# Performance work log

Hardware: AMD Instinct MI355X
Metric: run time of the kernel (lower is better)

## Reference

```python
import jax, jax.numpy as jnp
import numpy as np

DIM = 3072
HEADS = 24
HEAD_DIM = 128
INNER = HEADS * HEAD_DIM
EPS = 1e-6
B, IMG_LEN, TXT_LEN = 1, 2048, 512
S = IMG_LEN + TXT_LEN


def setup_inputs() -> dict:
    key = jax.random.key(0)
    ks = jax.random.split(key, 16)
    w = lambda k, shp: (jax.random.normal(k, shp, dtype=jnp.float32) * 0.02)
    return {
        "x": jax.random.normal(ks[0], (B, IMG_LEN, DIM), dtype=jnp.float32),
        "ctx": jax.random.normal(ks[1], (B, TXT_LEN, DIM), dtype=jnp.float32),
        "rope_cos": jax.random.uniform(ks[2], (S, HEAD_DIM), dtype=jnp.float32),
        "rope_sin": jax.random.uniform(ks[3], (S, HEAD_DIM), dtype=jnp.float32),
        "wq": w(ks[4], (INNER, DIM)),
        "wk": w(ks[5], (INNER, DIM)),
        "wv": w(ks[6], (INNER, DIM)),
        "gq": jnp.ones((HEAD_DIM,), jnp.float32),
        "gk": jnp.ones((HEAD_DIM,), jnp.float32),
        "wo": w(ks[7], (DIM, INNER)),
        "awq": w(ks[8], (INNER, DIM)),
        "awk": w(ks[9], (INNER, DIM)),
        "awv": w(ks[10], (INNER, DIM)),
        "agq": jnp.ones((HEAD_DIM,), jnp.float32),
        "agk": jnp.ones((HEAD_DIM,), jnp.float32),
        "awo": w(ks[11], (DIM, INNER)),
    }


def _rms_norm(t, g):
    # t: [b, s, h, d]; normalize over last dim
    var = jnp.mean(t * t, axis=-1, keepdims=True)
    return t * jax.lax.rsqrt(var + EPS) * g


def _heads(t):
    # [b, s, h*d] -> [b, s, h, d]
    b, s, _ = t.shape
    return t.reshape(b, s, HEADS, HEAD_DIM)


def _apply_rope(t, cos, sin):
    # t: [b, s, h, d]; cos/sin: [s, d] interleaved-pair layout (diffusers Flux style)
    b, s, h, d = t.shape
    x = t.reshape(b, s, h, d // 2, 2)
    rot = jnp.stack([-x[..., 1], x[..., 0]], axis=-1).reshape(b, s, h, d)
    c = cos[None, :, None, :]
    si = sin[None, :, None, :]
    return t * c + rot * si


def reference(x, ctx, rope_cos, rope_sin, wq, wk, wv, gq, gk, wo,
              awq, awk, awv, agq, agk, awo):
    # image-stream QKV + per-head RMSNorm on q,k
    q = _rms_norm(_heads(x @ wq.T), gq)
    k = _rms_norm(_heads(x @ wk.T), gk)
    v = _heads(x @ wv.T)
    # context-stream QKV
    qc = _rms_norm(_heads(ctx @ awq.T), agq)
    kc = _rms_norm(_heads(ctx @ awk.T), agk)
    vc = _heads(ctx @ awv.T)
    # joint streams: [ctx, img] ordering (out[:, :txt_len] is context)
    q = jnp.concatenate([qc, q], axis=1)
    k = jnp.concatenate([kc, k], axis=1)
    v = jnp.concatenate([vc, v], axis=1)
    q = _apply_rope(q, rope_cos, rope_sin)
    k = _apply_rope(k, rope_cos, rope_sin)
    # SDPA
    scale = 1.0 / jnp.sqrt(jnp.float32(HEAD_DIM))
    scores = jnp.einsum('bqhd,bkhd->bhqk', q, k) * scale
    probs = jax.nn.softmax(scores, axis=-1)
    out = jnp.einsum('bhqk,bkhd->bqhd', probs, v)
    out = out.reshape(out.shape[0], out.shape[1], INNER)
    img_out = out[:, TXT_LEN:] @ wo.T
    txt_out = out[:, :TXT_LEN] @ awo.T
    return (img_out, txt_out)
```

## Files before the change

kernel.cpp:

```cpp
#include <hip/hip_runtime.h>
#include <hip/hip_bf16.h>

#define DIMC 3072
#define NHEADS 24
#define HD 128
#define SEQ 2560
#define TXTLEN 512
#define IMGLEN 2048

using short8 = __attribute__((ext_vector_type(8))) short;
using f32x4  = __attribute__((ext_vector_type(4))) float;

static __device__ __forceinline__ float bf2f(unsigned short u) {
    unsigned v = ((unsigned)u) << 16;
    return __builtin_bit_cast(float, v);
}
static __device__ __forceinline__ unsigned short f2bf(float f) {
    unsigned u = __builtin_bit_cast(unsigned, f);
    return (unsigned short)((u + 0x7FFFu + ((u >> 16) & 1u)) >> 16);
}
static __device__ __forceinline__ void gload16(const void* g, void* l) {
    __builtin_amdgcn_global_load_lds((const __attribute__((address_space(1))) unsigned int*)g,
                                     (__attribute__((address_space(3))) unsigned int*)l,
                                     16, 0, 0);
}

struct C2 { const float* src[2]; size_t n8[2]; unsigned short* dst[2]; };
__global__ __launch_bounds__(256)
void castk2(C2 a)
{
    const int which = blockIdx.y;
    const size_t i = (size_t)blockIdx.x * 256 + threadIdx.x;
    if (i >= a.n8[which]) return;
    const float* in = a.src[which];
    unsigned short* out = a.dst[which];
    const float4 av = *reinterpret_cast<const float4*>(in + i * 8);
    const float4 bv = *reinterpret_cast<const float4*>(in + i * 8 + 4);
    short8 o;
    o[0] = (short)f2bf(av.x); o[1] = (short)f2bf(av.y);
    o[2] = (short)f2bf(av.z); o[3] = (short)f2bf(av.w);
    o[4] = (short)f2bf(bv.x); o[5] = (short)f2bf(bv.y);
    o[6] = (short)f2bf(bv.z); o[7] = (short)f2bf(bv.w);
    *reinterpret_cast<short8*>(out + i * 8) = o;
}

struct W8 { const float* src[8]; };
__global__ __launch_bounds__(256)
void castw(W8 a, unsigned short* __restrict__ dstbase, int n8, size_t wsz)
{
    const int i = blockIdx.x * 256 + threadIdx.x;
    if (i >= n8) return;
    const float* in = a.src[blockIdx.y];
    unsigned short* out = dstbase + (size_t)blockIdx.y * wsz;
    const float4 av = *reinterpret_cast<const float4*>(in + (size_t)i * 8);
    const float4 bv = *reinterpret_cast<const float4*>(in + (size_t)i * 8 + 4);
    short8 o;
    o[0] = (short)f2bf(av.x); o[1] = (short)f2bf(av.y);
    o[2] = (short)f2bf(av.z); o[3] = (short)f2bf(av.w);
    o[4] = (short)f2bf(bv.x); o[5] = (short)f2bf(bv.y);
    o[6] = (short)f2bf(bv.z); o[7] = (short)f2bf(bv.w);
    *reinterpret_cast<short8*>(out + (size_t)i * 8) = o;
}

struct QkvArgs {
    const unsigned short* A;
    const unsigned short* w0[3];
    const unsigned short* w1[3];
    unsigned short* c[3];
};

__global__ __launch_bounds__(256)
void gemm_qkv(QkvArgs args)
{
    __shared__ unsigned short As[3][128 * 32];
    __shared__ unsigned short Bs[3][128 * 32];

    const int bid = blockIdx.x;
    const int swz = (bid & 7) * 180 + (bid >> 3);
    const int bm = swz % 20;
    int bn = swz / 20;
    const int which = bn / 24; bn -= which * 24;

    const int rowbase = bm * 128, colbase = bn * 128;
    const unsigned short* __restrict__ A = args.A;
    const unsigned short* __restrict__ W = (rowbase < TXTLEN) ? args.w0[which] : args.w1[which];
    unsigned short* __restrict__ C = args.c[which];

    const int t = threadIdx.x, w = t >> 6, l = t & 63;
    const int lr = l & 15, lk = l >> 4;
    const int wr = (w >> 1) * 64, wc = (w & 1) * 64;

    f32x4 acc[4][4] = {};

    const int ssl = ((l & 3) ^ ((l >> 3) & 3)) * 8;
    const unsigned short* Ag = A + (size_t)(rowbase + w * 32 + (l >> 2)) * DIMC + ssl;
    const unsigned short* Wg = W + (size_t)(colbase + w * 32 + (l >> 2)) * DIMC + ssl;

    auto STAGE = [&](int buf, int k0) {
        gload16(Ag + k0,             &As[buf][w * 1024]);
        gload16(Ag + 16 * DIMC + k0, &As[buf][w * 1024 + 512]);
        gload16(Wg + k0,             &Bs[buf][w * 1024]);
        gload16(Wg + 16 * DIMC + k0, &Bs[buf][w * 1024 + 512]);
    };

    constexpr int NIT = DIMC / 32;
    STAGE(0, 0);
    STAGE(1, 32);

    const int rsl = (lk ^ ((lr >> 1) & 3)) * 8;
    int buf = 0;
    for (int it = 0; it < NIT; ++it) {
        asm volatile("s_waitcnt vmcnt(4)" ::: "memory");
        __builtin_amdgcn_s_barrier();
        asm volatile("" ::: "memory");

        {
            const int k2 = (it + 2 < NIT) ? (it + 2) : (NIT - 1);
            int b2 = buf + 2; if (b2 >= 3) b2 -= 3;
            STAGE(b2, k2 * 32);
        }

        short8 af[4], bf[4];
#pragma unroll
        for (int m = 0; m < 4; ++m)
            af[m] = *reinterpret_cast<const short8*>(&As[buf][(wr + m * 16 + lr) * 32 + rsl]);
#pragma unroll
        for (int n = 0; n < 4; ++n)
            bf[n] = *reinterpret_cast<const short8*>(&Bs[buf][(wc + n * 16 + lr) * 32 + rsl]);

        __builtin_amdgcn_s_setprio(1);
#pragma unroll
        for (int m = 0; m < 4; ++m)
#pragma unroll
            for (int n = 0; n < 4; ++n)
                acc[m][n] = __builtin_amdgcn_mfma_f32_16x16x32_bf16(af[m], bf[n], acc[m][n], 0, 0, 0);
        __builtin_amdgcn_s_setprio(0);

        buf = (buf + 1 == 3) ? 0 : buf + 1;
    }

#pragma unroll
    for (int m = 0; m < 4; ++m) {
#pragma unroll
        for (int r = 0; r < 4; ++r) {
            const int row = rowbase + wr + m * 16 + lk * 4 + r;
            unsigned short* crow = C + (size_t)row * DIMC + colbase + wc;
#pragma unroll
            for (int n = 0; n < 4; ++n)
                crow[n * 16 + lr] = f2bf(acc[m][n][r]);
        }
    }
}

__global__ __launch_bounds__(256)
void gemm_out(const unsigned short* __restrict__ A, const unsigned short* __restrict__ W0,
              const unsigned short* __restrict__ W1, float* __restrict__ Ctxt,
              float* __restrict__ Cimg)
{
    __shared__ unsigned short As[3][128 * 32];
    __shared__ unsigned short Bs[3][128 * 32];

    const int bid = blockIdx.x;
    const int swz = (bid & 7) * 60 + (bid >> 3);
    const int bm = swz % 20;
    const int bn = swz / 20;

    const int rowbase = bm * 128, colbase = bn * 128;
    const unsigned short* __restrict__ W = (rowbase < TXTLEN) ? W0 : W1;

    const int t = threadIdx.x, w = t >> 6, l = t & 63;
    const int lr = l & 15, lk = l >> 4;
    const int wr = (w >> 1) * 64, wc = (w & 1) * 64;

    f32x4 acc[4][4] = {};

    const int ssl = ((l & 3) ^ ((l >> 3) & 3)) * 8;
    const unsigned short* Ag = A + (size_t)(rowbase + w * 32 + (l >> 2)) * DIMC + ssl;
    const unsigned short* Wg = W + (size_t)(colbase + w * 32 + (l >> 2)) * DIMC + ssl;

    auto STAGE = [&](int buf, int k0) {
        gload16(Ag + k0,             &As[buf][w * 1024]);
        gload16(Ag + 16 * DIMC + k0, &As[buf][w * 1024 + 512]);
        gload16(Wg + k0,             &Bs[buf][w * 1024]);
        gload16(Wg + 16 * DIMC + k0, &Bs[buf][w * 1024 + 512]);
    };

    constexpr int NIT = DIMC / 32;
    STAGE(0, 0);
    STAGE(1, 32);

    const int rsl = (lk ^ ((lr >> 1) & 3)) * 8;
    int buf = 0;
    for (int it = 0; it < NIT; ++it) {
        asm volatile("s_waitcnt vmcnt(4)" ::: "memory");
        __builtin_amdgcn_s_barrier();
        asm volatile("" ::: "memory");

        {
            const int k2 = (it + 2 < NIT) ? (it + 2) : (NIT - 1);
            int b2 = buf + 2; if (b2 >= 3) b2 -= 3;
            STAGE(b2, k2 * 32);
        }

        short8 af[4], bf[4];
#pragma unroll
        for (int m = 0; m < 4; ++m)
            af[m] = *reinterpret_cast<const short8*>(&As[buf][(wr + m * 16 + lr) * 32 + rsl]);
#pragma unroll
        for (int n = 0; n < 4; ++n)
            bf[n] = *reinterpret_cast<const short8*>(&Bs[buf][(wc + n * 16 + lr) * 32 + rsl]);

        __builtin_amdgcn_s_setprio(1);
#pragma unroll
        for (int m = 0; m < 4; ++m)
#pragma unroll
            for (int n = 0; n < 4; ++n)
                acc[m][n] = __builtin_amdgcn_mfma_f32_16x16x32_bf16(af[m], bf[n], acc[m][n], 0, 0, 0);
        __builtin_amdgcn_s_setprio(0);

        buf = (buf + 1 == 3) ? 0 : buf + 1;
    }

    float* Cb; int rloc;
    if (rowbase < TXTLEN) { Cb = Ctxt; rloc = rowbase; }
    else                  { Cb = Cimg; rloc = rowbase - TXTLEN; }
#pragma unroll
    for (int m = 0; m < 4; ++m) {
#pragma unroll
        for (int r = 0; r < 4; ++r) {
            const int row = rloc + wr + m * 16 + lk * 4 + r;
            float* crow = Cb + (size_t)row * DIMC + colbase + wc;
#pragma unroll
            for (int n = 0; n < 4; ++n)
                crow[n * 16 + lr] = acc[m][n][r];
        }
    }
}

__global__ __launch_bounds__(256)
void normrope(unsigned short* __restrict__ Q, unsigned short* __restrict__ K,
              const float* __restrict__ gq, const float* __restrict__ gk,
              const float* __restrict__ agq, const float* __restrict__ agk,
              const float* __restrict__ rc, const float* __restrict__ rs)
{
    const int wid  = (blockIdx.x << 2) + (threadIdx.x >> 6);
    const int lane = threadIdx.x & 63;
    const int s = wid / NHEADS, h = wid - s * NHEADS;
    const bool img = (s >= TXTLEN);
    const float* gq_ = img ? gq : agq;
    const float* gk_ = img ? gk : agk;

    const size_t base = (size_t)s * DIMC + h * HD + lane * 2;
    const float2 c2  = *reinterpret_cast<const float2*>(rc + (size_t)s * HD + lane * 2);
    const float2 s2  = *reinterpret_cast<const float2*>(rs + (size_t)s * HD + lane * 2);
    const float2 gqv = *reinterpret_cast<const float2*>(gq_ + lane * 2);
    const float2 gkv = *reinterpret_cast<const float2*>(gk_ + lane * 2);

    {
        unsigned pr = *reinterpret_cast<unsigned*>(Q + base);
        float vx = bf2f((unsigned short)(pr & 0xffff));
        float vy = bf2f((unsigned short)(pr >> 16));
        float ss = vx * vx + vy * vy;
#pragma unroll
        for (int off = 1; off < 64; off <<= 1) ss += __shfl_xor(ss, off);
        const float rr = rsqrtf(ss * (1.f / HD) + 1e-6f);
        const float txv = vx * rr * gqv.x, tyv = vy * rr * gqv.y;
        const float qs = 0.08838834764831845f;
        const float ox = (txv * c2.x - tyv * s2.x) * qs;
        const float oy = (tyv * c2.y + txv * s2.y) * qs;
        *reinterpret_cast<unsigned*>(Q + base) = (unsigned)f2bf(ox) | ((unsigned)f2bf(oy) << 16);
    }
    {
        unsigned pr = *reinterpret_cast<unsigned*>(K + base);
        float vx = bf2f((unsigned short)(pr & 0xffff));
        float vy = bf2f((unsigned short)(pr >> 16));
        float ss = vx * vx + vy * vy;
#pragma unroll
        for (int off = 1; off < 64; off <<= 1) ss += __shfl_xor(ss, off);
        const float rr = rsqrtf(ss * (1.f / HD) + 1e-6f);
        const float txv = vx * rr * gkv.x, tyv = vy * rr * gkv.y;
        const float ox = txv * c2.x - tyv * s2.x;
        const float oy = tyv * c2.y + txv * s2.y;
        *reinterpret_cast<unsigned*>(K + base) = (unsigned)f2bf(ox) | ((unsigned)f2bf(oy) << 16);
    }
}

__global__ __launch_bounds__(256)
void transpose_v(const unsigned short* __restrict__ V, unsigned short* __restrict__ Vt)
{
    __shared__ unsigned short Ts[64][136];
    const int kt = blockIdx.x, h = blockIdx.y;
    const int t = threadIdx.x;
#pragma unroll
    for (int p = 0; p < 4; ++p) {
        const int row = p * 16 + (t >> 4);
        const int col = (t & 15) * 8;
        *reinterpret_cast<short8*>(&Ts[row][col]) =
            *reinterpret_cast<const short8*>(V + (size_t)(kt * 64 + row) * DIMC + h * HD + col);
    }
    __syncthreads();
    const int d = t >> 1, kh = t & 1;
    unsigned short* dst = Vt + (size_t)h * HD * SEQ + (size_t)d * SEQ + kt * 64 + kh * 32;
#pragma unroll
    for (int j4 = 0; j4 < 4; ++j4) {
        short8 o;
#pragma unroll
        for (int j = 0; j < 8; ++j) o[j] = (short)Ts[kh * 32 + j4 * 8 + j][d];
        *reinterpret_cast<short8*>(dst + j4 * 8) = o;
    }
}

__global__ __launch_bounds__(512)
void attn_mfma(const unsigned short* __restrict__ Q, const unsigned short* __restrict__ K,
               const unsigned short* __restrict__ Vt, unsigned short* __restrict__ O)
{
    __shared__ unsigned short Ks[2][64 * 128];
    __shared__ unsigned short Vs[2][128 * 64];
    __shared__ unsigned short Ps[8][16 * 64];

    const int bid = blockIdx.x;
    const int swz = (bid & 7) * 60 + (bid >> 3);
    const int bq = swz % 20;
    const int h  = swz / 20;

    const int t = threadIdx.x, w = t >> 6, l = t & 63;
    const int lr = l & 15, lk = l >> 4;
    const int q0 = bq * 128 + w * 16;

    short8 qf[4];
#pragma unroll
    for (int kk = 0; kk < 4; ++kk)
        qf[kk] = *reinterpret_cast<const short8*>(
            Q + (size_t)(q0 + lr) * DIMC + h * HD + kk * 32 + lk * 8);

    f32x4 oacc[8] = {};
    float mrow[4] = {-1e30f, -1e30f, -1e30f, -1e30f};
    float lrow[4] = {};

    const unsigned short* Kg[2];
    const unsigned short* Vg[2];
#pragma unroll
    for (int i = 0; i < 2; ++i) {
        const int kr = w * 8 + i * 4 + (l >> 4);
        Kg[i] = K + (size_t)kr * DIMC + h * HD + (((l & 15) ^ (kr & 7)) * 8);
        const int vr = w * 16 + i * 8 + (l >> 3);
        Vg[i] = Vt + (size_t)h * HD * SEQ + (size_t)vr * SEQ + (((l & 7) ^ (vr & 7)) * 8);
    }

    auto STAGE = [&](int buf, int kv0) {
#pragma unroll
        for (int i = 0; i < 2; ++i) {
            gload16(Kg[i] + (size_t)kv0 * DIMC, &Ks[buf][(w * 8 + i * 4) * 128]);
            gload16(Vg[i] + kv0,                &Vs[buf][(w * 16 + i * 8) * 64]);
        }
    };

    STAGE(0, 0);

    constexpr int NT = SEQ / 64;
    for (int kt = 0; kt < NT; ++kt) {
        const int buf = kt & 1;
        __syncthreads();
        if (kt + 1 < NT) STAGE(buf ^ 1, (kt + 1) * 64);

        f32x4 sf[4] = {};
        __builtin_amdgcn_s_setprio(1);
#pragma unroll
        for (int nf = 0; nf < 4; ++nf) {
            const int row = nf * 16 + lr;
            const int sw = (row & 7) << 3;
#pragma unroll
            for (int kk = 0; kk < 4; ++kk) {
                short8 bfr = *reinterpret_cast<const short8*>(
                    &Ks[buf][row * 128 + ((kk * 32 + lk * 8) ^ sw)]);
                sf[nf] = __builtin_amdgcn_mfma_f32_16x16x32_bf16(qf[kk], bfr, sf[nf], 0, 0, 0);
            }
        }
        __builtin_amdgcn_s_setprio(0);

        float mxr[4];
#pragma unroll
        for (int r = 0; r < 4; ++r) {
            float mx = fmaxf(fmaxf(sf[0][r], sf[1][r]), fmaxf(sf[2][r], sf[3][r]));
#pragma unroll
            for (int off = 1; off < 16; off <<= 1) mx = fmaxf(mx, __shfl_xor(mx, off));
            mxr[r] = mx;
        }
        const float need = fmaxf(fmaxf(mxr[0] - mrow[0], mxr[1] - mrow[1]),
                                 fmaxf(mxr[2] - mrow[2], mxr[3] - mrow[3]));
        if (!__all(need <= 8.0f)) {
#pragma unroll
            for (int r = 0; r < 4; ++r) {
                const float mn = fmaxf(mrow[r], mxr[r]);
                const float alpha = __expf(mrow[r] - mn);
                mrow[r] = mn;
                lrow[r] *= alpha;
#pragma unroll
                for (int nf = 0; nf < 8; ++nf) oacc[nf][r] *= alpha;
            }
        }
#pragma unroll
        for (int r = 0; r < 4; ++r) {
            float ps = 0.f;
#pragma unroll
            for (int nf = 0; nf < 4; ++nf) {
                const float p = __expf(sf[nf][r] - mrow[r]);
                sf[nf][r] = p;
                ps += p;
            }
#pragma unroll
            for (int off = 1; off < 16; off <<= 1) ps += __shfl_xor(ps, off);
            lrow[r] += ps;
        }

#pragma unroll
        for (int r = 0; r < 4; ++r) {
            const int prow = lk * 4 + r;
            const int sw = (prow & 7) << 3;
#pragma unroll
            for (int nf = 0; nf < 4; ++nf) {
                const int col = nf * 16 + lr;
                Ps[w][prow * 64 + (col ^ sw)] = f2bf(sf[nf][r]);
            }
        }

        __builtin_amdgcn_s_setprio(1);
#pragma unroll
        for (int ks = 0; ks < 2; ++ks) {
            short8 pa = *reinterpret_cast<const short8*>(
                &Ps[w][lr * 64 + ((ks * 32 + lk * 8) ^ ((lr & 7) << 3))]);
#pragma unroll
            for (int nf = 0; nf < 8; ++nf) {
                const int vrow = nf * 16 + lr;
                short8 vf = *reinterpret_cast<const short8*>(
                    &Vs[buf][vrow * 64 + ((ks * 32 + lk * 8) ^ ((vrow & 7) << 3))]);
                oacc[nf] = __builtin_amdgcn_mfma_f32_16x16x32_bf16(pa, vf, oacc[nf], 0, 0, 0);
            }
        }
        __builtin_amdgcn_s_setprio(0);
    }

    float inv[4];
#pragma unroll
    for (int r = 0; r < 4; ++r) inv[r] = 1.f / lrow[r];
#pragma unroll
    for (int nf = 0; nf < 8; ++nf)
#pragma unroll
        for (int r = 0; r < 4; ++r)
            O[(size_t)(q0 + lk * 4 + r) * DIMC + h * HD + nf * 16 + lr] = f2bf(oacc[nf][r] * inv[r]);
}

extern "C" void kernel_launch(void* const* d_in, const int* in_sizes, int n_in,
                              void* d_out, int out_size, void* d_ws, size_t ws_size,
                              hipStream_t stream)
{
    const float* x    = (const float*)d_in[0];
    const float* ctx  = (const float*)d_in[1];
    const float* rc   = (const float*)d_in[2];
    const float* rs   = (const float*)d_in[3];
    const float* wq   = (const float*)d_in[4];
    const float* wk   = (const float*)d_in[5];
    const float* wv   = (const float*)d_in[6];
    const float* gq   = (const float*)d_in[7];
    const float* gk   = (const float*)d_in[8];
    const float* wo   = (const float*)d_in[9];
    const float* awq  = (const float*)d_in[10];
    const float* awk  = (const float*)d_in[11];
    const float* awv  = (const float*)d_in[12];
    const float* agq  = (const float*)d_in[13];
    const float* agk  = (const float*)d_in[14];
    const float* awo  = (const float*)d_in[15];

    unsigned short* wsp = (unsigned short*)d_ws;
    const size_t SZ  = (size_t)SEQ * DIMC;
    const size_t WSZ = (size_t)DIMC * DIMC;
    unsigned short* XC  = wsp;
    unsigned short* Qb  = XC + SZ;
    unsigned short* Kb  = Qb + SZ;
    unsigned short* Vb  = Kb + SZ;
    unsigned short* Vtb = Vb + SZ;
    unsigned short* Ob  = Vtb + SZ;
    unsigned short* Wc  = Ob + SZ;

    {
        C2 c2a;
        c2a.src[0] = ctx; c2a.n8[0] = (size_t)TXTLEN * DIMC / 8; c2a.dst[0] = XC;
        c2a.src[1] = x;   c2a.n8[1] = (size_t)IMGLEN * DIMC / 8; c2a.dst[1] = XC + (size_t)TXTLEN * DIMC;
        const int maxb = (int)((c2a.n8[1] + 255) / 256);
        castk2<<<dim3(maxb, 2), dim3(256), 0, stream>>>(c2a);
    }
    {
        W8 w8;
        w8.src[0] = awq; w8.src[1] = wq; w8.src[2] = awk; w8.src[3] = wk;
        w8.src[4] = awv; w8.src[5] = wv; w8.src[6] = awo; w8.src[7] = wo;
        const int n8 = (int)(WSZ / 8);
        castw<<<dim3((n8 + 255) / 256, 8), dim3(256), 0, stream>>>(w8, Wc, n8, WSZ);
    }

    QkvArgs qa;
    qa.A = XC;
    qa.w0[0] = Wc + 0 * WSZ; qa.w1[0] = Wc + 1 * WSZ; qa.c[0] = Qb;
    qa.w0[1] = Wc + 2 * WSZ; qa.w1[1] = Wc + 3 * WSZ; qa.c[1] = Kb;
    qa.w0[2] = Wc + 4 * WSZ; qa.w1[2] = Wc + 5 * WSZ; qa.c[2] = Vb;
    gemm_qkv<<<dim3(1440), dim3(256), 0, stream>>>(qa);

    normrope<<<dim3(SEQ * NHEADS / 4), dim3(256), 0, stream>>>(Qb, Kb, gq, gk, agq, agk, rc, rs);

    transpose_v<<<dim3(SEQ / 64, NHEADS), dim3(256), 0, stream>>>(Vb, Vtb);

    attn_mfma<<<dim3(480), dim3(512), 0, stream>>>(Qb, Kb, Vtb, Ob);

    float* out = (float*)d_out;
    gemm_out<<<dim3(480), dim3(256), 0, stream>>>(
        Ob, Wc + 6 * WSZ, Wc + 7 * WSZ, out + (size_t)IMGLEN * DIMC, out);
}
```

Baseline: 532.3 us.

## Fuse fp32 weight cast into GEMM loaders, drop separate weight-cast kernel

Removes the standalone kernel that cast all eight fp32 weight matrices to bf16. The GEMM kernels now load fp32 weights straight into registers, convert them, and write bf16 to shared memory, using a register-prefetch pipeline two stages deep on top of the existing async A loads. This saves the extra write and re-read of the bf16 weight copies. In exchange every GEMM block reads fp32 weights (twice the bytes) and repeats the conversion many times across row tiles, while adding register pressure and VALU work in the main loop.

```diff
diff --git a/kernel.cpp b/kernel.cpp
--- a/kernel.cpp
+++ b/kernel.cpp
@@ -44,28 +44,117 @@
     *reinterpret_cast<short8*>(out + i * 8) = o;
 }
 
-struct W8 { const float* src[8]; };
-__global__ __launch_bounds__(256)
-void castw(W8 a, unsigned short* __restrict__ dstbase, int n8, size_t wsz)
-{
-    const int i = blockIdx.x * 256 + threadIdx.x;
-    if (i >= n8) return;
-    const float* in = a.src[blockIdx.y];
-    unsigned short* out = dstbase + (size_t)blockIdx.y * wsz;
-    const float4 av = *reinterpret_cast<const float4*>(in + (size_t)i * 8);
-    const float4 bv = *reinterpret_cast<const float4*>(in + (size_t)i * 8 + 4);
-    short8 o;
-    o[0] = (short)f2bf(av.x); o[1] = (short)f2bf(av.y);
-    o[2] = (short)f2bf(av.z); o[3] = (short)f2bf(av.w);
-    o[4] = (short)f2bf(bv.x); o[5] = (short)f2bf(bv.y);
-    o[6] = (short)f2bf(bv.z); o[7] = (short)f2bf(bv.w);
-    *reinterpret_cast<short8*>(out + (size_t)i * 8) = o;
-}
+#define GEMM_BODY(EMIT_EPILOGUE)                                                         \
+    const int t = threadIdx.x, w = t >> 6, l = t & 63;                                   \
+    const int lr = l & 15, lk = l >> 4;                                                  \
+    const int wr = (w >> 1) * 64, wc = (w & 1) * 64;                                     \
+    f32x4 acc[4][4] = {};                                                                \
+    const int ssl = ((l & 3) ^ ((l >> 3) & 3)) * 8;                                      \
+    const unsigned short* Ag = A + (size_t)(rowbase + w * 32 + (l >> 2)) * DIMC + ssl;   \
+    const float* Wg = W + (size_t)(colbase + w * 32 + (l >> 2)) * DIMC + (l & 3) * 8;    \
+    const int wa0 = (w * 32 + (l >> 2)) * 32 + ssl;                                      \
+    const int wa1 = wa0 + 512;                                                           \
+    auto STAGE_A = [&](int buf, int k0) {                                                \
+        gload16(Ag + k0,             &As[buf][w * 1024]);                                \
+        gload16(Ag + 16 * DIMC + k0, &As[buf][w * 1024 + 512]);                          \
+    };                                                                                   \
+    auto LOADW = [&](int k0, float4& a, float4& b, float4& c2, float4& d) {              \
+        a  = *reinterpret_cast<const float4*>(Wg + k0);                                  \
+        b  = *reinterpret_cast<const float4*>(Wg + k0 + 4);                              \
+        c2 = *reinterpret_cast<const float4*>(Wg + 16 * DIMC + k0);                      \
+        d  = *reinterpret_cast<const float4*>(Wg + 16 * DIMC + k0 + 4);                  \
+    };                                                                                   \
+    auto CVTW = [&](int buf, float4 a, float4 b, float4 c2, float4 d) {                  \
+        short8 s0, s1;                                                                   \
+        s0[0] = (short)f2bf(a.x);  s0[1] = (short)f2bf(a.y);                             \
+        s0[2] = (short)f2bf(a.z);  s0[3] = (short)f2bf(a.w);                             \
+        s0[4] = (short)f2bf(b.x);  s0[5] = (short)f2bf(b.y);                             \
+        s0[6] = (short)f2bf(b.z);  s0[7] = (short)f2bf(b.w);                             \
+        s1[0] = (short)f2bf(c2.x); s1[1] = (short)f2bf(c2.y);                            \
+        s1[2] = (short)f2bf(c2.z); s1[3] = (short)f2bf(c2.w);                            \
+        s1[4] = (short)f2bf(d.x);  s1[5] = (short)f2bf(d.y);                             \
+        s1[6] = (short)f2bf(d.z);  s1[7] = (short)f2bf(d.w);                             \
+        *reinterpret_cast<short8*>(&Bs[buf][wa0]) = s0;                                  \
+        *reinterpret_cast<short8*>(&Bs[buf][wa1]) = s1;                                  \
+    };                                                                                   \
+    constexpr int NIT = DIMC / 32;                                         \
+    float4 rA0, rA1, rA2, rA3, rB0, rB1, rB2, rB3;                                       \
+       \
+    LOADW(0,  rA0, rA1, rA2, rA3);                                                       \
+    LOADW(32, rB0, rB1, rB2, rB3);                                                       \
+    asm volatile("s_waitcnt vmcnt(4)" ::: "memory");                                     \
+    CVTW(0, rA0, rA1, rA2, rA3);                                                         \
+    asm volatile("s_waitcnt vmcnt(0)" ::: "memory");                                     \
+    CVTW(1, rB0, rB1, rB2, rB3);                                                         \
+    LOADW(64, rA0, rA1, rA2, rA3);                                                       \
+    STAGE_A(0, 0);                                                                       \
+    LOADW(96, rB0, rB1, rB2, rB3);                                                       \
+    STAGE_A(1, 32);                                                                      \
+    const int rsl = (lk ^ ((lr >> 1) & 3)) * 8;                                          \
+    int buf = 0;                                                                         \
+    for (int it = 0; it < NIT; it += 2) {                                                \
+                                             \
+        {                                                                                \
+            asm volatile("s_waitcnt vmcnt(6) lgkmcnt(0)" ::: "memory");                  \
+            __builtin_amdgcn_s_barrier();                                                \
+            asm volatile("" ::: "memory");                                               \
+            int b2 = buf + 2; if (b2 >= 3) b2 -= 3;                                      \
+            CVTW(b2, rA0, rA1, rA2, rA3);                                                \
+            const int k4 = ((it + 4 < NIT) ? it + 4 : NIT - 1) * 32;                     \
+            LOADW(k4, rA0, rA1, rA2, rA3);                                               \
+            const int k2 = ((it + 2 < NIT) ? it + 2 : NIT - 1) * 32;                     \
+            STAGE_A(b2, k2);                                                             \
+            short8 af[4], bf[4];                                                         \
+            _Pragma("unroll")                                                            \
+            for (int m = 0; m < 4; ++m)                                                  \
+                af[m] = *reinterpret_cast<const short8*>(&As[buf][(wr + m * 16 + lr) * 32 + rsl]); \
+            _Pragma("unroll")                                                            \
+            for (int n = 0; n < 4; ++n)                                                  \
+                bf[n] = *reinterpret_cast<const short8*>(&Bs[buf][(wc + n * 16 + lr) * 32 + rsl]); \
+            __builtin_amdgcn_s_setprio(1);                                               \
+            _Pragma("unroll")                                                            \
+            for (int m = 0; m < 4; ++m)                                                  \
+                _Pragma("unroll")                                                        \
+                for (int n = 0; n < 4; ++n)                                              \
+                    acc[m][n] = __builtin_amdgcn_mfma_f32_16x16x32_bf16(af[m], bf[n], acc[m][n], 0, 0, 0); \
+            __builtin_amdgcn_s_setprio(0);                                               \
+            buf = (buf + 1 == 3) ? 0 : buf + 1;                                          \
+        }                                                                                \
+                                              \
+        {                                                                                \
+            const int jt = it + 1;                                                       \
+            asm volatile("s_waitcnt vmcnt(6) lgkmcnt(0)" ::: "memory");                  \
+            __builtin_amdgcn_s_barrier();                                                \
+            asm volatile("" ::: "memory");                                               \
+            int b2 = buf + 2; if (b2 >= 3) b2 -= 3;                                      \
+            CVTW(b2, rB0, rB1, rB2, rB3);                                                \
+            const int k4 = ((jt + 4 < NIT) ? jt + 4 : NIT - 1) * 32;                     \
+            LOADW(k4, rB0, rB1, rB2, rB3);                                               \
+            const int k2 = ((jt + 2 < NIT) ? jt + 2 : NIT - 1) * 32;                     \
+            STAGE_A(b2, k2);                                                             \
+            short8 af[4], bf[4];                                                         \
+            _Pragma("unroll")                                                            \
+            for (int m = 0; m < 4; ++m)                                                  \
+                af[m] = *reinterpret_cast<const short8*>(&As[buf][(wr + m * 16 + lr) * 32 + rsl]); \
+            _Pragma("unroll")                                                            \
+            for (int n = 0; n < 4; ++n)                                                  \
+                bf[n] = *reinterpret_cast<const short8*>(&Bs[buf][(wc + n * 16 + lr) * 32 + rsl]); \
+            __builtin_amdgcn_s_setprio(1);                                               \
+            _Pragma("unroll")                                                            \
+            for (int m = 0; m < 4; ++m)                                                  \
+                _Pragma("unroll")                                                        \
+                for (int n = 0; n < 4; ++n)                                              \
+                    acc[m][n] = __builtin_amdgcn_mfma_f32_16x16x32_bf16(af[m], bf[n], acc[m][n], 0, 0, 0); \
+            __builtin_amdgcn_s_setprio(0);                                               \
+            buf = (buf + 1 == 3) ? 0 : buf + 1;                                          \
+        }                                                                                \
+    }                                                                                    \
+    EMIT_EPILOGUE
 
 struct QkvArgs {
     const unsigned short* A;
-    const unsigned short* w0[3];
-    const unsigned short* w1[3];
+    const float* w0[3];
+    const float* w1[3];
     unsigned short* c[3];
 };
 
@@ -83,78 +172,27 @@
 
     const int rowbase = bm * 128, colbase = bn * 128;
     const unsigned short* __restrict__ A = args.A;
-    const unsigned short* __restrict__ W = (rowbase < TXTLEN) ? args.w0[which] : args.w1[which];
+    const float* __restrict__ W = (rowbase < TXTLEN) ? args.w0[which] : args.w1[which];
     unsigned short* __restrict__ C = args.c[which];
 
-    const int t = threadIdx.x, w = t >> 6, l = t & 63;
-    const int lr = l & 15, lk = l >> 4;
-    const int wr = (w >> 1) * 64, wc = (w & 1) * 64;
-
-    f32x4 acc[4][4] = {};
-
-    const int ssl = ((l & 3) ^ ((l >> 3) & 3)) * 8;
-    const unsigned short* Ag = A + (size_t)(rowbase + w * 32 + (l >> 2)) * DIMC + ssl;
-    const unsigned short* Wg = W + (size_t)(colbase + w * 32 + (l >> 2)) * DIMC + ssl;
-
-    auto STAGE = [&](int buf, int k0) {
-        gload16(Ag + k0,             &As[buf][w * 1024]);
-        gload16(Ag + 16 * DIMC + k0, &As[buf][w * 1024 + 512]);
-        gload16(Wg + k0,             &Bs[buf][w * 1024]);
-        gload16(Wg + 16 * DIMC + k0, &Bs[buf][w * 1024 + 512]);
-    };
-
-    constexpr int NIT = DIMC / 32;
-    STAGE(0, 0);
-    STAGE(1, 32);
-
-    const int rsl = (lk ^ ((lr >> 1) & 3)) * 8;
-    int buf = 0;
-    for (int it = 0; it < NIT; ++it) {
-        asm volatile("s_waitcnt vmcnt(4)" ::: "memory");
-        __builtin_amdgcn_s_barrier();
-        asm volatile("" ::: "memory");
-
-        {
-            const int k2 = (it + 2 < NIT) ? (it + 2) : (NIT - 1);
-            int b2 = buf + 2; if (b2 >= 3) b2 -= 3;
-            STAGE(b2, k2 * 32);
-        }
-
-        short8 af[4], bf[4];
-#pragma unroll
-        for (int m = 0; m < 4; ++m)
-            af[m] = *reinterpret_cast<const short8*>(&As[buf][(wr + m * 16 + lr) * 32 + rsl]);
-#pragma unroll
-        for (int n = 0; n < 4; ++n)
-            bf[n] = *reinterpret_cast<const short8*>(&Bs[buf][(wc + n * 16 + lr) * 32 + rsl]);
-
-        __builtin_amdgcn_s_setprio(1);
-#pragma unroll
-        for (int m = 0; m < 4; ++m)
-#pragma unroll
-            for (int n = 0; n < 4; ++n)
-                acc[m][n] = __builtin_amdgcn_mfma_f32_16x16x32_bf16(af[m], bf[n], acc[m][n], 0, 0, 0);
-        __builtin_amdgcn_s_setprio(0);
-
-        buf = (buf + 1 == 3) ? 0 : buf + 1;
-    }
-
-#pragma unroll
-    for (int m = 0; m < 4; ++m) {
-#pragma unroll
-        for (int r = 0; r < 4; ++r) {
-            const int row = rowbase + wr + m * 16 + lk * 4 + r;
-            unsigned short* crow = C + (size_t)row * DIMC + colbase + wc;
-#pragma unroll
-            for (int n = 0; n < 4; ++n)
-                crow[n * 16 + lr] = f2bf(acc[m][n][r]);
-        }
-    }
+    GEMM_BODY(
+        _Pragma("unroll")
+        for (int m = 0; m < 4; ++m) {
+            _Pragma("unroll")
+            for (int r = 0; r < 4; ++r) {
+                const int row = rowbase + wr + m * 16 + lk * 4 + r;
+                unsigned short* crow = C + (size_t)row * DIMC + colbase + wc;
+                _Pragma("unroll")
+                for (int n = 0; n < 4; ++n)
+                    crow[n * 16 + lr] = f2bf(acc[m][n][r]);
+            }
+        }
+    )
 }
 
 __global__ __launch_bounds__(256)
-void gemm_out(const unsigned short* __restrict__ A, const unsigned short* __restrict__ W0,
-              const unsigned short* __restrict__ W1, float* __restrict__ Ctxt,
+void gemm_out(const unsigned short* __restrict__ A, const float* __restrict__ W0,
+              const float* __restrict__ W1, float* __restrict__ Ctxt,
               float* __restrict__ Cimg)
 {
     __shared__ unsigned short As[3][128 * 32];
@@ -166,75 +204,24 @@
     const int bn = swz / 20;
 
     const int rowbase = bm * 128, colbase = bn * 128;
-    const unsigned short* __restrict__ W = (rowbase < TXTLEN) ? W0 : W1;
-
-    const int t = threadIdx.x, w = t >> 6, l = t & 63;
-    const int lr = l & 15, lk = l >> 4;
-    const int wr = (w >> 1) * 64, wc = (w & 1) * 64;
-
-    f32x4 acc[4][4] = {};
-
-    const int ssl = ((l & 3) ^ ((l >> 3) & 3)) * 8;
-    const unsigned short* Ag = A + (size_t)(rowbase + w * 32 + (l >> 2)) * DIMC + ssl;
-    const unsigned short* Wg = W + (size_t)(colbase + w * 32 + (l >> 2)) * DIMC + ssl;
-
-    auto STAGE = [&](int buf, int k0) {
-        gload16(Ag + k0,             &As[buf][w * 1024]);
-        gload16(Ag + 16 * DIMC + k0, &As[buf][w * 1024 + 512]);
-        gload16(Wg + k0,             &Bs[buf][w * 1024]);
-        gload16(Wg + 16 * DIMC + k0, &Bs[buf][w * 1024 + 512]);
-    };
-
-    constexpr int NIT = DIMC / 32;
-    STAGE(0, 0);
-    STAGE(1, 32);
-
-    const int rsl = (lk ^ ((lr >> 1) & 3)) * 8;
-    int buf = 0;
-    for (int it = 0; it < NIT; ++it) {
-        asm volatile("s_waitcnt vmcnt(4)" ::: "memory");
-        __builtin_amdgcn_s_barrier();
-        asm volatile("" ::: "memory");
-
-        {
-            const int k2 = (it + 2 < NIT) ? (it + 2) : (NIT - 1);
-            int b2 = buf + 2; if (b2 >= 3) b2 -= 3;
-            STAGE(b2, k2 * 32);
-        }
-
-        short8 af[4], bf[4];
-#pragma unroll
-        for (int m = 0; m < 4; ++m)
-            af[m] = *reinterpret_cast<const short8*>(&As[buf][(wr + m * 16 + lr) * 32 + rsl]);
-#pragma unroll
-        for (int n = 0; n < 4; ++n)
-            bf[n] = *reinterpret_cast<const short8*>(&Bs[buf][(wc + n * 16 + lr) * 32 + rsl]);
-
-        __builtin_amdgcn_s_setprio(1);
-#pragma unroll
-        for (int m = 0; m < 4; ++m)
-#pragma unroll
-            for (int n = 0; n < 4; ++n)
-                acc[m][n] = __builtin_amdgcn_mfma_f32_16x16x32_bf16(af[m], bf[n], acc[m][n], 0, 0, 0);
-        __builtin_amdgcn_s_setprio(0);
-
-        buf = (buf + 1 == 3) ? 0 : buf + 1;
-    }
-
-    float* Cb; int rloc;
-    if (rowbase < TXTLEN) { Cb = Ctxt; rloc = rowbase; }
-    else                  { Cb = Cimg; rloc = rowbase - TXTLEN; }
-#pragma unroll
-    for (int m = 0; m < 4; ++m) {
-#pragma unroll
-        for (int r = 0; r < 4; ++r) {
-            const int row = rloc + wr + m * 16 + lk * 4 + r;
-            float* crow = Cb + (size_t)row * DIMC + colbase + wc;
-#pragma unroll
-            for (int n = 0; n < 4; ++n)
-                crow[n * 16 + lr] = acc[m][n][r];
-        }
-    }
+    const float* __restrict__ W = (rowbase < TXTLEN) ? W0 : W1;
+
+    GEMM_BODY(
+        float* Cb; int rloc;
+        if (rowbase < TXTLEN) { Cb = Ctxt; rloc = rowbase; }
+        else                  { Cb = Cimg; rloc = rowbase - TXTLEN; }
+        _Pragma("unroll")
+        for (int m = 0; m < 4; ++m) {
+            _Pragma("unroll")
+            for (int r = 0; r < 4; ++r) {
+                const int row = rloc + wr + m * 16 + lk * 4 + r;
+                float* crow = Cb + (size_t)row * DIMC + colbase + wc;
+                _Pragma("unroll")
+                for (int n = 0; n < 4; ++n)
+                    crow[n * 16 + lr] = acc[m][n][r];
+            }
+        }
+    )
 }
 
 __global__ __launch_bounds__(256)
@@ -473,14 +460,12 @@
 
     unsigned short* wsp = (unsigned short*)d_ws;
     const size_t SZ  = (size_t)SEQ * DIMC;
-    const size_t WSZ = (size_t)DIMC * DIMC;
     unsigned short* XC  = wsp;
     unsigned short* Qb  = XC + SZ;
     unsigned short* Kb  = Qb + SZ;
     unsigned short* Vb  = Kb + SZ;
     unsigned short* Vtb = Vb + SZ;
     unsigned short* Ob  = Vtb + SZ;
-    unsigned short* Wc  = Ob + SZ;
 
     {
         C2 c2a;
@@ -489,19 +474,12 @@
         const int maxb = (int)((c2a.n8[1] + 255) / 256);
         castk2<<<dim3(maxb, 2), dim3(256), 0, stream>>>(c2a);
     }
-    {
-        W8 w8;
-        w8.src[0] = awq; w8.src[1] = wq; w8.src[2] = awk; w8.src[3] = wk;
-        w8.src[4] = awv; w8.src[5] = wv; w8.src[6] = awo; w8.src[7] = wo;
-        const int n8 = (int)(WSZ / 8);
-        castw<<<dim3((n8 + 255) / 256, 8), dim3(256), 0, stream>>>(w8, Wc, n8, WSZ);
-    }
 
     QkvArgs qa;
     qa.A = XC;
-    qa.w0[0] = Wc + 0 * WSZ; qa.w1[0] = Wc + 1 * WSZ; qa.c[0] = Qb;
-    qa.w0[1] = Wc + 2 * WSZ; qa.w1[1] = Wc + 3 * WSZ; qa.c[1] = Kb;
-    qa.w0[2] = Wc + 4 * WSZ; qa.w1[2] = Wc + 5 * WSZ; qa.c[2] = Vb;
+    qa.w0[0] = awq; qa.w1[0] = wq; qa.c[0] = Qb;
+    qa.w0[1] = awk; qa.w1[1] = wk; qa.c[1] = Kb;
+    qa.w0[2] = awv; qa.w1[2] = wv; qa.c[2] = Vb;
     gemm_qkv<<<dim3(1440), dim3(256), 0, stream>>>(qa);
 
     normrope<<<dim3(SEQ * NHEADS / 4), dim3(256), 0, stream>>>(Qb, Kb, gq, gk, agq, agk, rc, rs);
@@ -512,5 +490,5 @@
 
     float* out = (float*)d_out;
     gemm_out<<<dim3(480), dim3(256), 0, stream>>>(
-        Ob, Wc + 6 * WSZ, Wc + 7 * WSZ, out + (size_t)IMGLEN * DIMC, out);
-}
+        Ob, awo, wo, out + (size_t)IMGLEN * DIMC, out);
+}
```

New measurement: 655.0 us. 1.23x slower.

## Enlarge QKV GEMM tile to 256x128 with 64x128 per-wave subtiles

Applied to the files above, without the earlier changes.

The QKV projection GEMM now uses 256-row by 128-column block tiles, so each wave computes a 64x128 subtile with 32 MFMA accumulators instead of 16. This halves the block count and is meant to raise arithmetic intensity per LDS fragment load and cut global traffic for the weight operand. The global-to-LDS staging and swizzle were rewritten for the new tile, the wait count was adjusted to 6 outstanding loads, and a launch bound of 2 blocks per SM was added. The cost is higher register and LDS use per block and fewer blocks for load balancing. The 512-row text segment still lines up with 256-row tiles, so the weight selection stays correct.

```diff
diff --git a/kernel.cpp b/kernel.cpp
--- a/kernel.cpp
+++ b/kernel.cpp
@@ -69,38 +69,42 @@
     unsigned short* c[3];
 };
 
-__global__ __launch_bounds__(256)
+__global__ __launch_bounds__(256, 2)
 void gemm_qkv(QkvArgs args)
 {
-    __shared__ unsigned short As[3][128 * 32];
+    __shared__ unsigned short As[3][256 * 32];
     __shared__ unsigned short Bs[3][128 * 32];
 
     const int bid = blockIdx.x;
-    const int swz = (bid & 7) * 180 + (bid >> 3);
-    const int bm = swz % 20;
-    int bn = swz / 20;
-    const int which = bn / 24; bn -= which * 24;
-
-    const int rowbase = bm * 128, colbase = bn * 128;
+    const int swz = (bid & 7) * 90 + (bid >> 3);
+    const int which = swz / 240;
+    const int rem = swz - which * 240;
+    const int bn = rem / 10;
+    const int bm = rem - bn * 10;
+
+    const int rowbase = bm * 256, colbase = bn * 128;
     const unsigned short* __restrict__ A = args.A;
     const unsigned short* __restrict__ W = (rowbase < TXTLEN) ? args.w0[which] : args.w1[which];
     unsigned short* __restrict__ C = args.c[which];
 
     const int t = threadIdx.x, w = t >> 6, l = t & 63;
     const int lr = l & 15, lk = l >> 4;
-    const int wr = (w >> 1) * 64, wc = (w & 1) * 64;
-
-    f32x4 acc[4][4] = {};
-
-    const int ssl = ((l & 3) ^ ((l >> 3) & 3)) * 8;
-    const unsigned short* Ag = A + (size_t)(rowbase + w * 32 + (l >> 2)) * DIMC + ssl;
-    const unsigned short* Wg = W + (size_t)(colbase + w * 32 + (l >> 2)) * DIMC + ssl;
+
+    f32x4 acc[4][8] = {};
+
+    const int srow = t >> 2;
+    const int ssl  = (((t & 3) ^ ((srow >> 1) & 3))) * 8;
+    const int dst0 = srow * 32 + (t & 3) * 8;
+    const unsigned short* Ag = A + (size_t)(rowbase + srow) * DIMC + ssl;
+    const unsigned short* Wg = W + (size_t)(colbase + srow) * DIMC + ssl;
 
     auto STAGE = [&](int buf, int k0) {
-        gload16(Ag + k0,             &As[buf][w * 1024]);
-        gload16(Ag + 16 * DIMC + k0, &As[buf][w * 1024 + 512]);
-        gload16(Wg + k0,             &Bs[buf][w * 1024]);
-        gload16(Wg + 16 * DIMC + k0, &Bs[buf][w * 1024 + 512]);
+#pragma unroll
+        for (int i = 0; i < 4; ++i)
+            gload16(Ag + (size_t)(i * 64) * DIMC + k0, &As[buf][i * 2048 + dst0]);
+#pragma unroll
+        for (int i = 0; i < 2; ++i)
+            gload16(Wg + (size_t)(i * 64) * DIMC + k0, &Bs[buf][i * 2048 + dst0]);
     };
 
     constexpr int NIT = DIMC / 32;
@@ -108,9 +112,10 @@
     STAGE(1, 32);
 
     const int rsl = (lk ^ ((lr >> 1) & 3)) * 8;
+    const int arow0 = w * 64 + lr;
     int buf = 0;
     for (int it = 0; it < NIT; ++it) {
-        asm volatile("s_waitcnt vmcnt(4)" ::: "memory");
+        asm volatile("s_waitcnt vmcnt(6)" ::: "memory");
         __builtin_amdgcn_s_barrier();
         asm volatile("" ::: "memory");
 
@@ -120,19 +125,19 @@
             STAGE(b2, k2 * 32);
         }
 
-        short8 af[4], bf[4];
+        short8 af[4], bf[8];
 #pragma unroll
         for (int m = 0; m < 4; ++m)
-            af[m] = *reinterpret_cast<const short8*>(&As[buf][(wr + m * 16 + lr) * 32 + rsl]);
-#pragma unroll
-        for (int n = 0; n < 4; ++n)
-            bf[n] = *reinterpret_cast<const short8*>(&Bs[buf][(wc + n * 16 + lr) * 32 + rsl]);
+            af[m] = *reinterpret_cast<const short8*>(&As[buf][(arow0 + m * 16) * 32 + rsl]);
+#pragma unroll
+        for (int n = 0; n < 8; ++n)
+            bf[n] = *reinterpret_cast<const short8*>(&Bs[buf][(n * 16 + lr) * 32 + rsl]);
 
         __builtin_amdgcn_s_setprio(1);
 #pragma unroll
         for (int m = 0; m < 4; ++m)
 #pragma unroll
-            for (int n = 0; n < 4; ++n)
+            for (int n = 0; n < 8; ++n)
                 acc[m][n] = __builtin_amdgcn_mfma_f32_16x16x32_bf16(af[m], bf[n], acc[m][n], 0, 0, 0);
         __builtin_amdgcn_s_setprio(0);
 
@@ -143,10 +148,10 @@
     for (int m = 0; m < 4; ++m) {
 #pragma unroll
         for (int r = 0; r < 4; ++r) {
-            const int row = rowbase + wr + m * 16 + lk * 4 + r;
-            unsigned short* crow = C + (size_t)row * DIMC + colbase + wc;
-#pragma unroll
-            for (int n = 0; n < 4; ++n)
+            const int row = rowbase + w * 64 + m * 16 + lk * 4 + r;
+            unsigned short* crow = C + (size_t)row * DIMC + colbase;
+#pragma unroll
+            for (int n = 0; n < 8; ++n)
                 crow[n * 16 + lr] = f2bf(acc[m][n][r]);
         }
     }
@@ -502,7 +507,7 @@
     qa.w0[0] = Wc + 0 * WSZ; qa.w1[0] = Wc + 1 * WSZ; qa.c[0] = Qb;
     qa.w0[1] = Wc + 2 * WSZ; qa.w1[1] = Wc + 3 * WSZ; qa.c[1] = Kb;
     qa.w0[2] = Wc + 4 * WSZ; qa.w1[2] = Wc + 5 * WSZ; qa.c[2] = Vb;
-    gemm_qkv<<<dim3(1440), dim3(256), 0, stream>>>(qa);
+    gemm_qkv<<<dim3(720), dim3(256), 0, stream>>>(qa);
 
     normrope<<<dim3(SEQ * NHEADS / 4), dim3(256), 0, stream>>>(Qb, Kb, gq, gk, agq, agk, rc, rs);
 
```

Measured after the change: 561.1 us. 5.4% more time.
